# Kernel optimization log

Hardware: AMD Instinct MI355X
Metric: run time of the kernel (lower is better)

The kernel has to match this reference:

```python
import jax, jax.numpy as jnp
import numpy as np
from jax import lax

# static dims (match init_kwargs)
B, F, C, H, W = 10, 64, 3, 180, 180   # batch=10 (hard-coded by reshape), arr_size frames
CH, OUT, NCLS = 64, 256, 5            # channel, out_size, len(ansmap)+1
K1, K2, POOL = 9, 5, 2                # second*diff, third, pool
EPS = 1e-5


def setup_inputs() -> dict:
    key = jax.random.key(0)
    ks = jax.random.split(key, 12)
    s = lambda k, shape: jax.random.normal(k, shape, dtype=jnp.float32) * 0.05
    return {
        "x": jax.random.normal(ks[0], (B, F, C, H, W), dtype=jnp.float32),
        "W1": s(ks[1], (CH, C, K1, K1)),
        "b1": s(ks[2], (CH,)),
        "W2": s(ks[3], (3, CH, K2, K2)),
        "b2": s(ks[4], (3,)),
        "gamma": jnp.ones((F,), jnp.float32),
        "beta": jnp.zeros((F,), jnp.float32),
        "Wih": s(ks[5], (3, OUT, 1)),
        "Whh": s(ks[6], (3, OUT, OUT)),
        "bih": s(ks[7], (3, OUT)),
        "bhh": s(ks[8], (3, OUT)),
        "Wl": s(ks[9], (NCLS, OUT)),
        "bl": s(ks[10], (NCLS,)),
    }


def _maxpool2(y):
    return lax.reduce_window(y, -jnp.inf, lax.max, (1, 1, POOL, POOL), (1, 1, POOL, POOL), 'VALID')


def reference(x, W1, b1, W2, b2, gamma, beta, Wih, Whh, bih, bhh, Wl, bl):
    # conv stack applied per frame; batch all B*F frames at once
    xc = x.reshape(B * F, C, H, W)
    y = lax.conv_general_dilated(xc, W1, (K1, K1), 'VALID') + b1[None, :, None, None]
    y = _maxpool2(jax.nn.relu(y))                      # [B*F, CH, 10, 10]
    y = lax.conv_general_dilated(y, W2, (K2, K2), 'VALID') + b2[None, :, None, None]
    y = _maxpool2(jax.nn.relu(y))                      # [B*F, 3, 1, 1]
    y = y.reshape(B, F, 3)

    # BatchNorm1d(arr_size) in train mode: normalize each of the F channels over (batch, length)
    mean = y.mean(axis=(0, 2), keepdims=True)
    var = y.var(axis=(0, 2), keepdims=True)
    y = (y - mean) / jnp.sqrt(var + EPS) * gamma[None, :, None] + beta[None, :, None]

    # per-sample reorder of the 3 channels by (max - min) range over time
    t = y.transpose(0, 2, 1)                           # [B, 3, F]
    rng = t.max(-1) - t.min(-1)                        # [B, 3]
    perm = jnp.argsort(rng, axis=1)                    # [B, 3]
    ts = jnp.take_along_axis(t, perm[:, :, None], axis=1)  # [B, 3, F]

    # rank r goes through RNN r; vmap the scan over the 3 RNNs
    seqs = ts.transpose(1, 2, 0)[..., None]            # [3, F, B, 1]

    def rnn_last(seq, wih, whh, bi, bh):               # seq: [F, B, 1]
        def step(h, xt):
            return jnp.tanh(xt @ wih.T + bi + h @ whh.T + bh), None
        h, _ = lax.scan(step, jnp.zeros((B, OUT), seq.dtype), seq)
        return h                                       # last hidden == output at t=-1

    lasts = jax.vmap(rnn_last)(seqs, Wih, Whh, bih, bhh)  # [3, B, OUT]
    avg = lasts.mean(axis=0)                           # AvgPool2d((3,1)) + Flatten -> [B, OUT]
    return avg @ Wl.T + bl                             # [B, NCLS]
```

## Files before the change

### kernel.cpp

```cpp
#include <hip/hip_runtime.h>

typedef __attribute__((ext_vector_type(8))) short bf16x8;
typedef __attribute__((ext_vector_type(4))) float f32x4;

#define MFMA16(a,b,c) __builtin_amdgcn_mfma_f32_16x16x32_bf16((a),(b),(c),0,0,0)

#define AS1 __attribute__((address_space(1)))
#define AS3 __attribute__((address_space(3)))
__device__ __forceinline__ void async16(void* lds, const void* g){
  __builtin_amdgcn_global_load_lds((const AS1 unsigned int*)g, (AS3 unsigned int*)lds, 16, 0, 0);
}

__device__ __forceinline__ unsigned short f2bf(float f){
  unsigned int u = __float_as_uint(f);
  unsigned int r = (u + 0x7fffu + ((u>>16)&1u)) >> 16;
  return (unsigned short)r;
}
__device__ __forceinline__ float bf2f(unsigned short h){
  return __uint_as_float(((unsigned int)h)<<16);
}
__device__ __forceinline__ float tanh_fast(float x){
  float e = __expf(2.f*x);
  return 1.f - 2.f/(e + 1.f);
}

#define WS_W1H   0u
#define WS_W1L   32768u
#define WS_WHHH  65536u
#define WS_WHHL  458752u
#define WS_Y1    851968u
#define WS_Y2    17235968u
#define WS_LAST  17255936u

__global__ __launch_bounds__(256) void k_prep(const float* __restrict__ W1,
                                              const float* __restrict__ Whh,
                                              unsigned short* __restrict__ w1h,
                                              unsigned short* __restrict__ w1l,
                                              unsigned short* __restrict__ whh_h,
                                              unsigned short* __restrict__ whh_l){
  int t = blockIdx.x*256 + threadIdx.x;
  if (t < 2048){
    int l = t & 63, kt = (t>>6)&7, mt = t>>9;
    int co = mt*16 + (l&15);
    int k0 = kt*32 + ((l>>4)<<3);
    bf16x8 hv, lv;
    #pragma unroll
    for (int j=0;j<8;j++){
      int k = k0 + j;
      float v = (k < 243) ? W1[co*243 + k] : 0.f;
      unsigned short h = f2bf(v);
      unsigned short lo = f2bf(v - bf2f(h));
      hv[j] = (short)h; lv[j] = (short)lo;
    }
    *(bf16x8*)(w1h + (size_t)t*8) = hv;
    *(bf16x8*)(w1l + (size_t)t*8) = lv;
  } else if (t < 2048 + 24576){
    int u = t - 2048;
    int l = u & 63, kt = (u>>6)&7, nt = (u>>9)&15, rnn = u>>13;
    int o = nt*16 + (l&15);
    int k0 = kt*32 + ((l>>4)<<3);
    const float* src = Whh + ((size_t)rnn*256 + o)*256;
    bf16x8 hv, lv;
    #pragma unroll
    for (int j=0;j<8;j++){
      float v = src[k0 + j];
      unsigned short h = f2bf(v);
      unsigned short lo = f2bf(v - bf2f(h));
      hv[j] = (short)h; lv[j] = (short)lo;
    }
    *(bf16x8*)(whh_h + (size_t)u*8) = hv;
    *(bf16x8*)(whh_l + (size_t)u*8) = lv;
  }
}

__global__ __launch_bounds__(256) void k_conv1(const float* __restrict__ x,
                                               const float* __restrict__ b1,
                                               const unsigned short* __restrict__ w1h,
                                               const unsigned short* __restrict__ w1l,
                                               float* __restrict__ y1){
  __shared__ __align__(16) char smem[20480];
  int fr = blockIdx.x/10, g = blockIdx.x%10;
  int t = threadIdx.x, w = t>>6, l = t&63;

  bf16x8 ah[8], al[8];
  #pragma unroll
  for (int kt=0;kt<8;kt++){
    size_t fi = (((size_t)(w*8+kt))*64 + l)*8;
    ah[kt] = *(const bf16x8*)(w1h+fi);
    al[kt] = *(const bf16x8*)(w1l+fi);
  }
  float bias[4];
  #pragma unroll
  for (int reg=0;reg<4;reg++) bias[reg] = b1[w*16 + ((l>>4)<<2) + reg];

  const float4* xb = (const float4*)x + (size_t)fr*24300;
  int rowbase = g*18;

  float4 rv[5]; int pp[5], kk[5], kxv[5]; bool okv[5];
  #pragma unroll
  for (int ii=0; ii<5; ii++){
    int i = t + (ii<<8);
    okv[ii] = (i < 1215);
    int c = i/405, rem = i - c*405;
    int ky = rem/45, quad = rem - ky*45;
    int col0 = quad<<2;
    int ox = (col0*57)>>9;
    kxv[ii] = col0 - 9*ox;
    pp[ii] = ox;
    kk[ii] = c*81 + ky*9;
    int gi = c*8100 + (rowbase + ky)*45 + quad;
    rv[ii] = okv[ii] ? xb[gi] : (float4){0.f,0.f,0.f,0.f};
  }
  for (int i=t; i<260; i+=256){
    int p = i/13, k = 243 + (i - p*13);
    int off = ((p<<9)+(k<<1)) ^ ((p&7)<<4);
    *(unsigned short*)(smem+off) = 0;
    *(unsigned short*)(smem+10240+off) = 0;
  }
  #pragma unroll
  for (int ii=0; ii<5; ii++){
    if (okv[ii]){
      int p = pp[ii], kx = kxv[ii];
      float vv[4] = {rv[ii].x, rv[ii].y, rv[ii].z, rv[ii].w};
      #pragma unroll
      for (int q=0;q<4;q++){
        int k = kk[ii] + kx;
        int off = ((p<<9)+(k<<1)) ^ ((p&7)<<4);
        unsigned int u = __float_as_uint(vv[q]);
        *(unsigned short*)(smem+off) = (unsigned short)(u>>16);
        float lof = vv[q] - __uint_as_float(u & 0xffff0000u);
        *(unsigned short*)(smem+10240+off) = (unsigned short)(__float_as_uint(lof)>>16);
        kx++; if (kx==9){ kx=0; p++; }
      }
    }
  }
  __syncthreads();

  #pragma unroll
  for (int ii=0; ii<5; ii++){
    int i = t + (ii<<8);
    int c = i/405, rem = i - c*405;
    int ky = rem/45, quad = rem - ky*45;
    int gi = c*8100 + (rowbase + 9 + ky)*45 + quad;
    rv[ii] = okv[ii] ? xb[gi] : (float4){0.f,0.f,0.f,0.f};
  }

  int m = l&15, colb = (l>>4)<<4;
  int p0 = m, p1 = 4+m;
  int sw0 = (p0&7)<<4, sw1 = (p1&7)<<4;
  f32x4 acc0 = (f32x4){0.f,0.f,0.f,0.f}, acc1 = acc0;
  #pragma unroll
  for (int kt=0;kt<8;kt++){
    int off0 = ((p0<<9)+(kt<<6)+colb) ^ sw0;
    int off1 = ((p1<<9)+(kt<<6)+colb) ^ sw1;
    bf16x8 bh0 = *(const bf16x8*)(smem+off0);
    bf16x8 bl0 = *(const bf16x8*)(smem+10240+off0);
    bf16x8 bh1 = *(const bf16x8*)(smem+off1);
    bf16x8 bl1 = *(const bf16x8*)(smem+10240+off1);
    acc0 = MFMA16(ah[kt], bh0, acc0);
    acc0 = MFMA16(ah[kt], bl0, acc0);
    acc0 = MFMA16(al[kt], bh0, acc0);
    acc1 = MFMA16(ah[kt], bh1, acc1);
    acc1 = MFMA16(ah[kt], bl1, acc1);
    acc1 = MFMA16(al[kt], bh1, acc1);
  }
  float vA0[4], vA1[4];
  #pragma unroll
  for (int reg=0;reg<4;reg++){
    float v0 = fmaxf(acc0[reg]+bias[reg], 0.f);
    vA0[reg] = fmaxf(v0, __shfl_xor(v0,1));
    float v1 = fmaxf(acc1[reg]+bias[reg], 0.f);
    vA1[reg] = fmaxf(v1, __shfl_xor(v1,1));
  }
  __syncthreads();

  #pragma unroll
  for (int ii=0; ii<5; ii++){
    if (okv[ii]){
      int p = pp[ii], kx = kxv[ii];
      float vv[4] = {rv[ii].x, rv[ii].y, rv[ii].z, rv[ii].w};
      #pragma unroll
      for (int q=0;q<4;q++){
        int k = kk[ii] + kx;
        int off = ((p<<9)+(k<<1)) ^ ((p&7)<<4);
        unsigned int u = __float_as_uint(vv[q]);
        *(unsigned short*)(smem+off) = (unsigned short)(u>>16);
        float lof = vv[q] - __uint_as_float(u & 0xffff0000u);
        *(unsigned short*)(smem+10240+off) = (unsigned short)(__float_as_uint(lof)>>16);
        kx++; if (kx==9){ kx=0; p++; }
      }
    }
  }
  __syncthreads();

  acc0 = (f32x4){0.f,0.f,0.f,0.f}; acc1 = acc0;
  #pragma unroll
  for (int kt=0;kt<8;kt++){
    int off0 = ((p0<<9)+(kt<<6)+colb) ^ sw0;
    int off1 = ((p1<<9)+(kt<<6)+colb) ^ sw1;
    bf16x8 bh0 = *(const bf16x8*)(smem+off0);
    bf16x8 bl0 = *(const bf16x8*)(smem+10240+off0);
    bf16x8 bh1 = *(const bf16x8*)(smem+off1);
    bf16x8 bl1 = *(const bf16x8*)(smem+10240+off1);
    acc0 = MFMA16(ah[kt], bh0, acc0);
    acc0 = MFMA16(ah[kt], bl0, acc0);
    acc0 = MFMA16(al[kt], bh0, acc0);
    acc1 = MFMA16(ah[kt], bh1, acc1);
    acc1 = MFMA16(ah[kt], bl1, acc1);
    acc1 = MFMA16(al[kt], bh1, acc1);
  }
  size_t ybase = (size_t)fr*6400 + g*10;
  #pragma unroll
  for (int reg=0;reg<4;reg++){
    int co = w*16 + ((l>>4)<<2) + reg;
    float v0 = fmaxf(acc0[reg]+bias[reg], 0.f);
    v0 = fmaxf(v0, __shfl_xor(v0,1));
    float r0 = fmaxf(vA0[reg], v0);
    float v1 = fmaxf(acc1[reg]+bias[reg], 0.f);
    v1 = fmaxf(v1, __shfl_xor(v1,1));
    float r1 = fmaxf(vA1[reg], v1);
    if ((m&1)==0){
      y1[ybase + co*100 + (m>>1)] = r0;
      if (m >= 12)
        y1[ybase + co*100 + ((4+m)>>1)] = r1;
    }
  }
}

__global__ __launch_bounds__(256) void k_conv2(const float* __restrict__ y1,
                                               const float* __restrict__ W2,
                                               const float* __restrict__ b2,
                                               float* __restrict__ y2){
  __shared__ __align__(16) float yl[6400];
  __shared__ __align__(16) float w2s[4800];
  int fr = blockIdx.x, t = threadIdx.x;
  const float4* src = (const float4*)(y1 + (size_t)fr*6400);
  for (int i=t;i<1600;i+=256) async16(((float4*)yl) + i, (const void*)(src + i));
  for (int i=t;i<1200;i+=256) async16(((float4*)w2s) + i, (const void*)(((const float4*)W2) + i));
  __syncthreads();
  if (t < 192){
    int o = t>>4, l16 = t&15;
    int ch = o>>2, pos = o&3;
    int oy = pos>>1, ox = pos&1;
    float s = 0.f;
    for (int i=0;i<100;i++){
      int k = l16 + (i<<4);
      int ci = k/25; int r = k - ci*25; int ky = r/5, kx = r - ky*5;
      s += yl[ci*100 + (5*oy+ky)*10 + 5*ox + kx] * w2s[ch*1600 + k];
    }
    #pragma unroll
    for (int d=1; d<16; d<<=1) s += __shfl_xor(s, d);
    float v = fmaxf(s + b2[ch], 0.f);
    v = fmaxf(v, __shfl_xor(v, 16));
    v = fmaxf(v, __shfl_xor(v, 32));
    if ((t&63)==0) y2[fr*3 + (t>>6)] = v;
  }
}

__global__ __launch_bounds__(512) void k_rnn(const unsigned short* __restrict__ whh_h,
                                             const unsigned short* __restrict__ whh_l,
                                             const float* __restrict__ y2,
                                             const float* __restrict__ gamma,
                                             const float* __restrict__ beta,
                                             const float* __restrict__ Wih,
                                             const float* __restrict__ bih,
                                             const float* __restrict__ bhh,
                                             float* __restrict__ lasts){
  __shared__ __align__(16) char hsm[36864];
  float* yl   = (float*)hsm;
  float* af   = (float*)(hsm + 7680);
  float* bfv  = (float*)(hsm + 7936);
  float* rngL = (float*)(hsm + 8192);
  int*   perm = (int*)(hsm + 8320);
  float* tsb  = (float*)(hsm + 8448);
  float* seqL = (float*)(hsm + 32768);
  int rnn = blockIdx.x;
  int t = threadIdx.x, w = t>>6, l = t&63;

  bf16x8 Bh[2][8], Bl[2][8];
  #pragma unroll
  for (int q=0;q<2;q++){
    int nt = 2*w + q;
    #pragma unroll
    for (int kt=0;kt<8;kt++){
      size_t fi = (((((size_t)rnn*16 + nt)*8) + kt)*64 + l)*8;
      Bh[q][kt] = *(const bf16x8*)(whh_h + fi);
      Bl[q][kt] = *(const bf16x8*)(whh_l + fi);
    }
  }
  int o0 = (2*w)*16 + (l&15), o1 = o0 + 16;
  float wih0 = Wih[rnn*256 + o0], wih1 = Wih[rnn*256 + o1];
  float bs0 = bih[rnn*256+o0] + bhh[rnn*256+o0];
  float bs1 = bih[rnn*256+o1] + bhh[rnn*256+o1];

  for (int i=t;i<1920;i+=512) yl[i] = y2[i];
  __syncthreads();
  if (t < 64){
    float mu = 0.f;
    for (int b=0;b<10;b++)
      for (int ch=0;ch<3;ch++) mu += yl[(b*64 + t)*3 + ch];
    mu *= (1.f/30.f);
    float v = 0.f;
    for (int b=0;b<10;b++)
      for (int ch=0;ch<3;ch++){ float d = yl[(b*64+t)*3+ch] - mu; v += d*d; }
    v *= (1.f/30.f);
    float rs = rsqrtf(v + 1e-5f);
    float a = gamma[t]*rs;
    af[t] = a; bfv[t] = beta[t] - mu*a;
  }
  __syncthreads();
  if (t < 30){
    int b = t/3, ch = t - b*3;
    float mx = -1e30f, mn = 1e30f;
    for (int f=0; f<64; f++){
      float v = yl[(b*64+f)*3+ch]*af[f] + bfv[f];
      tsb[(b*3+ch)*64 + f] = v;
      mx = fmaxf(mx, v); mn = fminf(mn, v);
    }
    rngL[b*3+ch] = mx - mn;
  }
  __syncthreads();
  if (t < 10){
    #pragma unroll
    for (int ch=0; ch<3; ch++){
      float rc = rngL[t*3+ch];
      int rank = 0;
      #pragma unroll
      for (int c2=0; c2<3; c2++){
        float r2 = rngL[t*3+c2];
        if (r2 < rc || (r2 == rc && c2 < ch)) rank++;
      }
      perm[t*3+rank] = ch;
    }
  }
  __syncthreads();
  for (int i=t;i<1024;i+=512){
    int step = i>>4, b = i&15;
    float v = 0.f;
    if (b < 10){ int p = perm[b*3 + rnn]; v = tsb[(b*3+p)*64 + step]; }
    seqL[i] = v;
  }
  __syncthreads();

  float4 z4 = {0.f,0.f,0.f,0.f};
  for (int i=t; i<1024; i+=512) ((float4*)hsm)[i] = z4;
  __syncthreads();
  int arow = l&15, colb = (l>>4)<<4, sw = (arow&7)<<4;
  int b_base = (l>>4)<<2;
  for (int step=0; step<64; step++){
    char* cur = hsm + ((step&1)<<14);
    char* nxt = hsm + (((step+1)&1)<<14);
    f32x4 p0=(f32x4){0,0,0,0}, q0=p0, r0=p0, p1=p0, q1=p0, r1=p0;
    #pragma unroll
    for (int kt=0; kt<8; kt++){
      int off = ((arow<<9) + (kt<<6) + colb) ^ sw;
      bf16x8 ahv = *(const bf16x8*)(cur + off);
      bf16x8 alv = *(const bf16x8*)(cur + 8192 + off);
      p0 = MFMA16(ahv, Bh[0][kt], p0);
      q0 = MFMA16(ahv, Bl[0][kt], q0);
      r0 = MFMA16(alv, Bh[0][kt], r0);
      p1 = MFMA16(ahv, Bh[1][kt], p1);
      q1 = MFMA16(ahv, Bl[1][kt], q1);
      r1 = MFMA16(alv, Bh[1][kt], r1);
    }
    float4 sx = *(const float4*)(seqL + (step<<4) + b_base);
    float sxa[4] = {sx.x, sx.y, sx.z, sx.w};
    #pragma unroll
    for (int reg=0; reg<4; reg++){
      int b = b_base + reg;
      float a0 = (p0[reg] + q0[reg]) + r0[reg];
      float a1 = (p1[reg] + q1[reg]) + r1[reg];
      float h0 = tanh_fast(a0 + sxa[reg]*wih0 + bs0);
      float h1 = tanh_fast(a1 + sxa[reg]*wih1 + bs1);
      int wsw = (b&7)<<4;
      int off0 = ((b<<9) + (o0<<1)) ^ wsw;
      int off1 = ((b<<9) + (o1<<1)) ^ wsw;
      unsigned int u0 = __float_as_uint(h0);
      unsigned int u1 = __float_as_uint(h1);
      *(unsigned short*)(nxt + off0) = (unsigned short)(u0>>16);
      float l0 = h0 - __uint_as_float(u0 & 0xffff0000u);
      *(unsigned short*)(nxt + 8192 + off0) = (unsigned short)(__float_as_uint(l0)>>16);
      *(unsigned short*)(nxt + off1) = (unsigned short)(u1>>16);
      float l1 = h1 - __uint_as_float(u1 & 0xffff0000u);
      *(unsigned short*)(nxt + 8192 + off1) = (unsigned short)(__float_as_uint(l1)>>16);
      if (step == 63){
        lasts[((size_t)rnn*16 + b)*256 + o0] = h0;
        lasts[((size_t)rnn*16 + b)*256 + o1] = h1;
      }
    }
    __syncthreads();
  }
}

__global__ __launch_bounds__(512) void k_head(const float* __restrict__ lasts,
                                              const float* __restrict__ Wl,
                                              const float* __restrict__ bl,
                                              float* __restrict__ out){
  int t = threadIdx.x;
  if (t < 400){
    int oidx = t>>3, l8 = t&7;
    int b = oidx/5, c = oidx - b*5;
    float s = 0.f;
    for (int i=0;i<32;i++){
      int o = (l8<<5) + i;
      float avg = (lasts[(size_t)(0*16+b)*256+o] + lasts[(size_t)(1*16+b)*256+o]
                 + lasts[(size_t)(2*16+b)*256+o]) * (1.f/3.f);
      s += avg * Wl[c*256 + o];
    }
    #pragma unroll
    for (int d=1; d<8; d<<=1) s += __shfl_xor(s, d);
    if (l8 == 0) out[oidx] = s + bl[c];
  }
}

extern "C" void kernel_launch(void* const* d_in, const int* in_sizes, int n_in,
                              void* d_out, int out_size, void* d_ws, size_t ws_size,
                              hipStream_t stream){
  const float* x    = (const float*)d_in[0];
  const float* W1   = (const float*)d_in[1];
  const float* b1   = (const float*)d_in[2];
  const float* W2   = (const float*)d_in[3];
  const float* b2   = (const float*)d_in[4];
  const float* gamma= (const float*)d_in[5];
  const float* beta = (const float*)d_in[6];
  const float* Wih  = (const float*)d_in[7];
  const float* Whh  = (const float*)d_in[8];
  const float* bih  = (const float*)d_in[9];
  const float* bhh  = (const float*)d_in[10];
  const float* Wl   = (const float*)d_in[11];
  const float* bl   = (const float*)d_in[12];
  char* ws = (char*)d_ws;
  unsigned short* w1h  = (unsigned short*)(ws + WS_W1H);
  unsigned short* w1l  = (unsigned short*)(ws + WS_W1L);
  unsigned short* whhh = (unsigned short*)(ws + WS_WHHH);
  unsigned short* whhl = (unsigned short*)(ws + WS_WHHL);
  float* y1   = (float*)(ws + WS_Y1);
  float* y2   = (float*)(ws + WS_Y2);
  float* last = (float*)(ws + WS_LAST);

  hipLaunchKernelGGL(k_prep,  dim3(104),  dim3(256), 0, stream, W1, Whh, w1h, w1l, whhh, whhl);
  hipLaunchKernelGGL(k_conv1, dim3(6400), dim3(256), 0, stream, x, b1, w1h, w1l, y1);
  hipLaunchKernelGGL(k_conv2, dim3(640),  dim3(256), 0, stream, y1, W2, b2, y2);
  hipLaunchKernelGGL(k_rnn,   dim3(3),    dim3(512), 0, stream, whhh, whhl, y2, gamma, beta, Wih, bih, bhh, last);
  hipLaunchKernelGGL(k_head,  dim3(1),    dim3(512), 0, stream, last, Wl, bl, (float*)d_out);
}
```

Measured before the change: 204.3 us.

## Reorder conv1 K dimension into 8-wide chunks for vectorized LDS im2col writes

Reorders the conv1 reduction dimension so each group of 8 consecutive K entries is the 8 kx taps of one (c,ky) row, with the ninth tap gathered into extra chunks. Weights are permuted to match in the prep kernel. Each thread can then write whole 16-byte chunks of hi/lo bf16 into LDS with perm packing, replacing scalar 2-byte scattered stores and swizzle math. Global loads become scalar strided float reads instead of float4, which may raise load instruction count, and the swizzle removal may reintroduce LDS bank conflicts.

```diff
diff --git a/kernel.cpp b/kernel.cpp
--- a/kernel.cpp
+++ b/kernel.cpp
@@ -31,6 +31,7 @@
 #define WS_Y1    851968u
 #define WS_Y2    17235968u
 #define WS_LAST  17255936u
+
 
 __global__ __launch_bounds__(256) void k_prep(const float* __restrict__ W1,
                                               const float* __restrict__ Whh,
@@ -42,12 +43,17 @@
   if (t < 2048){
     int l = t & 63, kt = (t>>6)&7, mt = t>>9;
     int co = mt*16 + (l&15);
-    int k0 = kt*32 + ((l>>4)<<3);
+    int o = (kt*32 + ((l>>4)<<3)) >> 3;
     bf16x8 hv, lv;
     #pragma unroll
     for (int j=0;j<8;j++){
-      int k = k0 + j;
-      float v = (k < 243) ? W1[co*243 + k] : 0.f;
+      float v = 0.f;
+      if (o < 27){
+        v = W1[co*243 + o*9 + j];
+      } else if (o < 31){
+        int idx = (o-27)*8 + j;
+        if (idx < 27) v = W1[co*243 + idx*9 + 8];
+      }
       unsigned short h = f2bf(v);
       unsigned short lo = f2bf(v - bf2f(h));
       hv[j] = (short)h; lv[j] = (short)lo;
@@ -73,6 +79,45 @@
   }
 }
 
+__device__ __forceinline__ void load_chunk(const float* __restrict__ xf, int rowbase,
+                                           int ch, float* __restrict__ f){
+  int o = (ch*205)>>12;
+  int p = ch - 20*o;
+  if (o < 27){
+    int c = (o*57)>>9;
+    int ky = o - 9*c;
+    const float* b = xf + c*32400 + (rowbase+ky)*180 + 9*p;
+    #pragma unroll
+    for (int j=0;j<8;j++) f[j] = b[j];
+  } else if (o < 31){
+    #pragma unroll
+    for (int j=0;j<8;j++){
+      int idx = (o-27)*8 + j;
+      int cc = (idx*57)>>9;
+      int kky = idx - 9*cc;
+      f[j] = (idx<27) ? xf[cc*32400 + (rowbase+kky)*180 + 9*p + 8] : 0.f;
+    }
+  } else {
+    #pragma unroll
+    for (int j=0;j<8;j++) f[j] = 0.f;
+  }
+}
+
+__device__ __forceinline__ void write_chunk(char* __restrict__ smem, int ch,
+                                            const float* __restrict__ f){
+  unsigned int hw[4], lw[4];
+  #pragma unroll
+  for (int i=0;i<4;i++){
+    unsigned int ua = __float_as_uint(f[2*i]), ub = __float_as_uint(f[2*i+1]);
+    float la = f[2*i]   - __uint_as_float(ua & 0xffff0000u);
+    float lb = f[2*i+1] - __uint_as_float(ub & 0xffff0000u);
+    hw[i] = __builtin_amdgcn_perm(ub, ua, 0x07060302u);
+    lw[i] = __builtin_amdgcn_perm(__float_as_uint(lb), __float_as_uint(la), 0x07060302u);
+  }
+  *(uint4*)(smem + ch*16)         = make_uint4(hw[0],hw[1],hw[2],hw[3]);
+  *(uint4*)(smem + 10240 + ch*16) = make_uint4(lw[0],lw[1],lw[2],lw[3]);
+}
+
 __global__ __launch_bounds__(256) void k_conv1(const float* __restrict__ x,
                                                const float* __restrict__ b1,
                                                const unsigned short* __restrict__ w1h,
@@ -81,6 +126,13 @@
   __shared__ __align__(16) char smem[20480];
   int fr = blockIdx.x/10, g = blockIdx.x%10;
   int t = threadIdx.x, w = t>>6, l = t&63;
+  const float* xf = x + (size_t)fr*97200;
+  int rb = g*18;
+
+  float f0[8], f1[8], f2[8];
+  load_chunk(xf, rb, t,      f0);
+  load_chunk(xf, rb, t+256,  f1);
+  if (t < 128) load_chunk(xf, rb, t+512, f2);
 
   bf16x8 ah[8], al[8];
   #pragma unroll
@@ -93,66 +145,22 @@
   #pragma unroll
   for (int reg=0;reg<4;reg++) bias[reg] = b1[w*16 + ((l>>4)<<2) + reg];
 
-  const float4* xb = (const float4*)x + (size_t)fr*24300;
-  int rowbase = g*18;
-
-  float4 rv[5]; int pp[5], kk[5], kxv[5]; bool okv[5];
-  #pragma unroll
-  for (int ii=0; ii<5; ii++){
-    int i = t + (ii<<8);
-    okv[ii] = (i < 1215);
-    int c = i/405, rem = i - c*405;
-    int ky = rem/45, quad = rem - ky*45;
-    int col0 = quad<<2;
-    int ox = (col0*57)>>9;
-    kxv[ii] = col0 - 9*ox;
-    pp[ii] = ox;
-    kk[ii] = c*81 + ky*9;
-    int gi = c*8100 + (rowbase + ky)*45 + quad;
-    rv[ii] = okv[ii] ? xb[gi] : (float4){0.f,0.f,0.f,0.f};
-  }
-  for (int i=t; i<260; i+=256){
-    int p = i/13, k = 243 + (i - p*13);
-    int off = ((p<<9)+(k<<1)) ^ ((p&7)<<4);
-    *(unsigned short*)(smem+off) = 0;
-    *(unsigned short*)(smem+10240+off) = 0;
-  }
-  #pragma unroll
-  for (int ii=0; ii<5; ii++){
-    if (okv[ii]){
-      int p = pp[ii], kx = kxv[ii];
-      float vv[4] = {rv[ii].x, rv[ii].y, rv[ii].z, rv[ii].w};
-      #pragma unroll
-      for (int q=0;q<4;q++){
-        int k = kk[ii] + kx;
-        int off = ((p<<9)+(k<<1)) ^ ((p&7)<<4);
-        unsigned int u = __float_as_uint(vv[q]);
-        *(unsigned short*)(smem+off) = (unsigned short)(u>>16);
-        float lof = vv[q] - __uint_as_float(u & 0xffff0000u);
-        *(unsigned short*)(smem+10240+off) = (unsigned short)(__float_as_uint(lof)>>16);
-        kx++; if (kx==9){ kx=0; p++; }
-      }
-    }
-  }
-  __syncthreads();
-
-  #pragma unroll
-  for (int ii=0; ii<5; ii++){
-    int i = t + (ii<<8);
-    int c = i/405, rem = i - c*405;
-    int ky = rem/45, quad = rem - ky*45;
-    int gi = c*8100 + (rowbase + 9 + ky)*45 + quad;
-    rv[ii] = okv[ii] ? xb[gi] : (float4){0.f,0.f,0.f,0.f};
-  }
-
-  int m = l&15, colb = (l>>4)<<4;
-  int p0 = m, p1 = 4+m;
-  int sw0 = (p0&7)<<4, sw1 = (p1&7)<<4;
+  write_chunk(smem, t,     f0);
+  write_chunk(smem, t+256, f1);
+  if (t < 128) write_chunk(smem, t+512, f2);
+  __syncthreads();
+
+  load_chunk(xf, rb+9, t,      f0);
+  load_chunk(xf, rb+9, t+256,  f1);
+  if (t < 128) load_chunk(xf, rb+9, t+512, f2);
+
+  int m = l&15;
+  int fb = ((l>>4)*320) + m*16;
   f32x4 acc0 = (f32x4){0.f,0.f,0.f,0.f}, acc1 = acc0;
   #pragma unroll
   for (int kt=0;kt<8;kt++){
-    int off0 = ((p0<<9)+(kt<<6)+colb) ^ sw0;
-    int off1 = ((p1<<9)+(kt<<6)+colb) ^ sw1;
+    int off0 = fb + kt*1280;
+    int off1 = off0 + 64;
     bf16x8 bh0 = *(const bf16x8*)(smem+off0);
     bf16x8 bl0 = *(const bf16x8*)(smem+10240+off0);
     bf16x8 bh1 = *(const bf16x8*)(smem+off1);
@@ -174,30 +182,16 @@
   }
   __syncthreads();
 
-  #pragma unroll
-  for (int ii=0; ii<5; ii++){
-    if (okv[ii]){
-      int p = pp[ii], kx = kxv[ii];
-      float vv[4] = {rv[ii].x, rv[ii].y, rv[ii].z, rv[ii].w};
-      #pragma unroll
-      for (int q=0;q<4;q++){
-        int k = kk[ii] + kx;
-        int off = ((p<<9)+(k<<1)) ^ ((p&7)<<4);
-        unsigned int u = __float_as_uint(vv[q]);
-        *(unsigned short*)(smem+off) = (unsigned short)(u>>16);
-        float lof = vv[q] - __uint_as_float(u & 0xffff0000u);
-        *(unsigned short*)(smem+10240+off) = (unsigned short)(__float_as_uint(lof)>>16);
-        kx++; if (kx==9){ kx=0; p++; }
-      }
-    }
-  }
+  write_chunk(smem, t,     f0);
+  write_chunk(smem, t+256, f1);
+  if (t < 128) write_chunk(smem, t+512, f2);
   __syncthreads();
 
   acc0 = (f32x4){0.f,0.f,0.f,0.f}; acc1 = acc0;
   #pragma unroll
   for (int kt=0;kt<8;kt++){
-    int off0 = ((p0<<9)+(kt<<6)+colb) ^ sw0;
-    int off1 = ((p1<<9)+(kt<<6)+colb) ^ sw1;
+    int off0 = fb + kt*1280;
+    int off1 = off0 + 64;
     bf16x8 bh0 = *(const bf16x8*)(smem+off0);
     bf16x8 bl0 = *(const bf16x8*)(smem+10240+off0);
     bf16x8 bh1 = *(const bf16x8*)(smem+off1);
```

Result: faster. 180.4 us (-11.7%).
